# Optimization experiments

Hardware: AMD Instinct MI355X
Metric: run time of the kernel (lower is better)

## Reference

```python
import jax, jax.numpy as jnp
import numpy as np

BSZ, SEQ, HID, OUT = 64, 1024, 1024, 1024


def setup_inputs() -> dict:
    key = jax.random.key(0)
    k1, k2, k3, k4, k5 = jax.random.split(key, 5)
    hidden = jax.random.normal(k1, (BSZ, HID), dtype=jnp.float32)
    encoder_outs = jax.random.normal(k2, (BSZ, SEQ, OUT), dtype=jnp.float32)
    src_lens = jax.random.randint(k3, (BSZ,), 1, SEQ + 1)  # valid lengths in [1, SEQ]
    # nn.Linear weights (PyTorch stores W as [out_features, in_features])
    W1 = jax.random.normal(k4, (OUT, HID), dtype=jnp.float32) / np.sqrt(HID)
    W2 = jax.random.normal(k5, (OUT, HID + OUT), dtype=jnp.float32) / np.sqrt(HID + OUT)
    return {"hidden": hidden, "encoder_outs": encoder_outs, "src_lens": src_lens,
            "W1": W1, "W2": W2}


def reference(hidden, encoder_outs, src_lens, W1, W2):
    # x = l1(hidden): [bsz, out]
    x = hidden @ W1.T
    # att_score = bmm(encoder_outs, x[..., None]).squeeze(-1).T : [seq, bsz]
    att_score = jnp.einsum("bsd,bd->sb", encoder_outs, x)
    seq = encoder_outs.shape[1]
    # seq_mask transposed: [seq, bsz]
    seq_mask = (jnp.arange(seq)[None, :] < src_lens[:, None]).T
    # masked_att = mask * score; then exact-zero entries (masked OR true zeros) -> -1e10
    masked_att = seq_mask * att_score
    masked_att = jnp.where(masked_att == 0, jnp.float32(-1e10), masked_att)
    attn_scores = jax.nn.softmax(masked_att, axis=0)  # softmax over seq dim
    # context = sum_s attn[s,b] * enc[b,s,d] : [bsz, out]
    ctx = jnp.einsum("sb,bsd->bd", attn_scores, encoder_outs)
    out = jnp.tanh(jnp.concatenate((ctx, hidden), axis=1) @ W2.T)
    return out, attn_scores
```

## Files before the change

### kernel.cpp

```cpp
#include <hip/hip_runtime.h>
#include <math.h>

#define BSZ 64
#define SEQ 1024
#define HID 1024
#define DOUT 1024
#define SPLIT 16
#define CHUNK (SEQ/SPLIT)

typedef float f32x4 __attribute__((ext_vector_type(4)));


__global__ __launch_bounds__(256) void k_gemv_hid(const float* __restrict__ hidden,
                                                  const float* __restrict__ W1,
                                                  const float* __restrict__ W2,
                                                  float* __restrict__ xpart,
                                                  float* __restrict__ outpart) {
    __shared__ float tile[128 * 65];
    int t = threadIdx.x, lane = t & 63, wave = t >> 6;
    int k0 = blockIdx.y * 128;
#pragma unroll
    for (int p = 0; p < 8; ++p) {
        int b = p * 8 + (t >> 5), l5 = t & 31;
        f32x4 h = *(const f32x4*)&hidden[b * 1024 + k0 + l5 * 4];
        tile[(l5 * 4 + 0) * 65 + b] = h.x;
        tile[(l5 * 4 + 1) * 65 + b] = h.y;
        tile[(l5 * 4 + 2) * 65 + b] = h.z;
        tile[(l5 * 4 + 3) * 65 + b] = h.w;
    }
    __syncthreads();
    bool isX = blockIdx.x < 64;
    int cg = isX ? blockIdx.x : blockIdx.x - 64;
    int c_base = cg * 16 + (wave << 2);
    const float* w0p = isX ? (W1 + (size_t)c_base * 1024 + k0)
                           : (W2 + (size_t)c_base * 2048 + 1024 + k0);
    size_t ldw = isX ? 1024 : 2048;
    float acc[4] = {0.f, 0.f, 0.f, 0.f};
    for (int k = 0; k < 128; k += 4) {
        float v0 = tile[(k + 0) * 65 + lane];
        float v1 = tile[(k + 1) * 65 + lane];
        float v2 = tile[(k + 2) * 65 + lane];
        float v3 = tile[(k + 3) * 65 + lane];
#pragma unroll
        for (int oi = 0; oi < 4; ++oi) {
            f32x4 w = *(const f32x4*)&w0p[oi * ldw + k];
            acc[oi] += w.x * v0 + w.y * v1 + w.z * v2 + w.w * v3;
        }
    }
    float* dst = isX ? (xpart + (size_t)blockIdx.y * 65536)
                     : (outpart + (size_t)(8 + blockIdx.y) * 65536);
#pragma unroll
    for (int oi = 0; oi < 4; ++oi)
        dst[(size_t)lane * 1024 + c_base + oi] = acc[oi];
}

__global__ __launch_bounds__(256, 4) void k_score(const float* __restrict__ enc,
                                                  const float* __restrict__ xpart,
                                                  const int* __restrict__ src_lens,
                                                  float* __restrict__ scoresG,
                                                  float* __restrict__ ctx_part,
                                                  float* __restrict__ ml_part) {
    int b = blockIdx.y, chunk = blockIdx.x;
    int t = threadIdx.x, lane = t & 63, wave = t >> 6;
    __shared__ f32x4 accbuf[4 * 256];
    __shared__ float mbuf[4], lbuf[4];

    f32x4 xv[4];
#pragma unroll
    for (int i = 0; i < 4; ++i) {
        f32x4 s = (f32x4)0.f;
#pragma unroll
        for (int ks = 0; ks < 8; ++ks)
            s += ((const f32x4*)(xpart + (size_t)ks * 65536 + (size_t)b * 1024))[i * 64 + lane];
        xv[i] = s;
    }
    int len = src_lens[b];
    int s_wave0 = chunk * CHUNK + wave * 16;
    const float* encb = enc + ((size_t)b << 20);

    float m_run = -3.0e38f, l_run = 0.f;
    f32x4 acc[4];
#pragma unroll
    for (int i = 0; i < 4; ++i) acc[i] = (f32x4)0.f;

#pragma unroll 1
    for (int g = 0; g < 4; ++g) {
        int sbase = s_wave0 + g * 4;
        if (sbase >= len) {
            if (lane == 0) {
#pragma unroll
                for (int j = 0; j < 4; ++j) scoresG[(sbase + j) * BSZ + b] = -1.0e10f;
            }
            continue;
        }
        f32x4 e[4][4];
#pragma unroll
        for (int j = 0; j < 4; ++j) {
            const f32x4* row4 = (const f32x4*)(encb + (size_t)(sbase + j) * DOUT);
#pragma unroll
            for (int i = 0; i < 4; ++i) e[j][i] = row4[i * 64 + lane];
        }
        float d0 = 0.f, d1 = 0.f, d2 = 0.f, d3 = 0.f;
#pragma unroll
        for (int i = 0; i < 4; ++i) {
            d0 += e[0][i].x * xv[i].x + e[0][i].y * xv[i].y + e[0][i].z * xv[i].z + e[0][i].w * xv[i].w;
            d1 += e[1][i].x * xv[i].x + e[1][i].y * xv[i].y + e[1][i].z * xv[i].z + e[1][i].w * xv[i].w;
            d2 += e[2][i].x * xv[i].x + e[2][i].y * xv[i].y + e[2][i].z * xv[i].z + e[2][i].w * xv[i].w;
            d3 += e[3][i].x * xv[i].x + e[3][i].y * xv[i].y + e[3][i].z * xv[i].z + e[3][i].w * xv[i].w;
        }
#pragma unroll
        for (int off = 32; off > 0; off >>= 1) {
            d0 += __shfl_xor(d0, off, 64);
            d1 += __shfl_xor(d1, off, 64);
            d2 += __shfl_xor(d2, off, 64);
            d3 += __shfl_xor(d3, off, 64);
        }
        float v0 = (sbase + 0 < len) ? d0 : 0.f; if (v0 == 0.f) v0 = -1.0e10f;
        float v1 = (sbase + 1 < len) ? d1 : 0.f; if (v1 == 0.f) v1 = -1.0e10f;
        float v2 = (sbase + 2 < len) ? d2 : 0.f; if (v2 == 0.f) v2 = -1.0e10f;
        float v3 = (sbase + 3 < len) ? d3 : 0.f; if (v3 == 0.f) v3 = -1.0e10f;
        if (lane == 0) {
            scoresG[(sbase + 0) * BSZ + b] = v0;
            scoresG[(sbase + 1) * BSZ + b] = v1;
            scoresG[(sbase + 2) * BSZ + b] = v2;
            scoresG[(sbase + 3) * BSZ + b] = v3;
        }
        float msub = fmaxf(fmaxf(v0, v1), fmaxf(v2, v3));
        float m_new = fmaxf(m_run, msub);
        float scale = __expf(m_run - m_new);
        float p0 = __expf(v0 - m_new), p1 = __expf(v1 - m_new);
        float p2 = __expf(v2 - m_new), p3 = __expf(v3 - m_new);
        l_run = l_run * scale + (p0 + p1 + p2 + p3);
        m_run = m_new;
#pragma unroll
        for (int i = 0; i < 4; ++i)
            acc[i] = acc[i] * scale + p0 * e[0][i] + p1 * e[1][i] + p2 * e[2][i] + p3 * e[3][i];
    }

#pragma unroll
    for (int i = 0; i < 4; ++i) accbuf[wave * 256 + i * 64 + lane] = acc[i];
    if (lane == 0) { mbuf[wave] = m_run; lbuf[wave] = l_run; }
    __syncthreads();
    float M = fmaxf(fmaxf(mbuf[0], mbuf[1]), fmaxf(mbuf[2], mbuf[3]));
    float w0 = __expf(mbuf[0] - M), w1 = __expf(mbuf[1] - M);
    float w2 = __expf(mbuf[2] - M), w3 = __expf(mbuf[3] - M);
    f32x4 tot = accbuf[t] * w0 + accbuf[256 + t] * w1 + accbuf[512 + t] * w2 + accbuf[768 + t] * w3;
    ((f32x4*)(ctx_part + ((size_t)(b * SPLIT + chunk) << 10)))[t] = tot;
    if (t == 0) {
        float Lt = lbuf[0] * w0 + lbuf[1] * w1 + lbuf[2] * w2 + lbuf[3] * w3;
        ml_part[(b * SPLIT + chunk) * 2] = M;
        ml_part[(b * SPLIT + chunk) * 2 + 1] = Lt;
    }
}

__global__ __launch_bounds__(256) void k_reduce_attn(const float* __restrict__ ctx_part,
                                                     const float* __restrict__ ml_part,
                                                     const float* __restrict__ scoresG,
                                                     float* __restrict__ ctxT,
                                                     float* __restrict__ outAttn) {
    int b = blockIdx.x >> 2, q = blockIdx.x & 3, t = threadIdx.x;
    float M = -3.0e38f;
#pragma unroll
    for (int c = 0; c < SPLIT; ++c) M = fmaxf(M, ml_part[(b * SPLIT + c) * 2]);
    float L = 0.f;
    float wgt[SPLIT];
#pragma unroll
    for (int c = 0; c < SPLIT; ++c) {
        float e = __expf(ml_part[(b * SPLIT + c) * 2] - M);
        wgt[c] = e;
        L += ml_part[(b * SPLIT + c) * 2 + 1] * e;
    }
    float inv = 1.f / L;
    int d = q * 256 + t;
    float acc = 0.f;
#pragma unroll
    for (int c = 0; c < SPLIT; ++c)
        acc += wgt[c] * ctx_part[((size_t)(b * SPLIT + c) << 10) + d];
    ctxT[d * BSZ + b] = acc * inv;
    outAttn[d * BSZ + b] = __expf(scoresG[d * BSZ + b] - M) * inv;
}

__global__ __launch_bounds__(256) void k_out_part(const float* __restrict__ W2,
                                                  const float* __restrict__ ctxT,
                                                  float* __restrict__ outpart) {
    __shared__ float tile[128 * 64];
    int t = threadIdx.x, lane = t & 63, wave = t >> 6;
    int k0 = blockIdx.y * 128;
    int c_base = blockIdx.x * 16 + (wave << 2);
    {
        const f32x4* src = (const f32x4*)(ctxT + k0 * 64);
        f32x4* dst = (f32x4*)tile;
#pragma unroll
        for (int i = 0; i < 8; ++i) dst[t + i * 256] = src[t + i * 256];
    }
    __syncthreads();
    float acc[4] = {0.f, 0.f, 0.f, 0.f};
    for (int k = 0; k < 128; k += 4) {
        float v0 = tile[(k + 0) * 64 + lane];
        float v1 = tile[(k + 1) * 64 + lane];
        float v2 = tile[(k + 2) * 64 + lane];
        float v3 = tile[(k + 3) * 64 + lane];
#pragma unroll
        for (int oi = 0; oi < 4; ++oi) {
            f32x4 w = *(const f32x4*)&W2[(size_t)(c_base + oi) * 2048 + k0 + k];
            acc[oi] += w.x * v0 + w.y * v1 + w.z * v2 + w.w * v3;
        }
    }
#pragma unroll
    for (int oi = 0; oi < 4; ++oi)
        outpart[(size_t)blockIdx.y * 65536 + (size_t)lane * 1024 + c_base + oi] = acc[oi];
}

__global__ void k_out_reduce(const float* __restrict__ outpart, float* __restrict__ out) {
    int idx = blockIdx.x * 256 + threadIdx.x;
    float s = 0.f;
#pragma unroll
    for (int ks = 0; ks < 16; ++ks) s += outpart[(size_t)ks * 65536 + idx];
    out[idx] = tanhf(s);
}

extern "C" void kernel_launch(void* const* d_in, const int* in_sizes, int n_in,
                              void* d_out, int out_size, void* d_ws, size_t ws_size,
                              hipStream_t stream) {
    const float* hidden   = (const float*)d_in[0];
    const float* enc      = (const float*)d_in[1];
    const int*   src_lens = (const int*)d_in[2];
    const float* W1       = (const float*)d_in[3];
    const float* W2       = (const float*)d_in[4];
    float* out     = (float*)d_out;
    float* outAttn = out + 65536;

    float* ws       = (float*)d_ws;
    float* scoresG  = ws;
    float* ctxT     = ws + 65536;
    float* ctx_part = ws + 131072;
    float* ml_part  = ws + 1179648;
    float* xpart    = ws + 1181696;
    float* outpart  = ws + 1705984;

    k_gemv_hid<<<dim3(128, 8), 256, 0, stream>>>(hidden, W1, W2, xpart, outpart);
    k_score<<<dim3(SPLIT, BSZ), 256, 0, stream>>>(enc, xpart, src_lens, scoresG, ctx_part, ml_part);
    k_reduce_attn<<<256, 256, 0, stream>>>(ctx_part, ml_part, scoresG, ctxT, outAttn);
    k_out_part<<<dim3(64, 8), 256, 0, stream>>>(W2, ctxT, outpart);
    k_out_reduce<<<256, 256, 0, stream>>>(outpart, out);
}
```

Before: 72.11 us.

## Fuse output GEMV with tanh and concat, drop split-K reduce kernel

Removes the hidden-part of the W2 GEMV from the first kernel. The reduce-attention kernel now writes a transposed concat of context and hidden. A new single k_out kernel runs the full K=2048 dot per output column and applies tanh directly, which removes the split-K partial buffer and the separate reduce launch. The score kernel now loops only over valid groups, and masked attention entries are written as zero in the reduce kernel instead of storing -1e10 scores. The cost is that each k_out block walks the whole K range serially with only 256 blocks, which lowers parallelism on the W2 pass.

```diff
diff --git a/kernel.cpp b/kernel.cpp
--- a/kernel.cpp
+++ b/kernel.cpp
@@ -11,11 +11,9 @@
 typedef float f32x4 __attribute__((ext_vector_type(4)));
 
 
-__global__ __launch_bounds__(256) void k_gemv_hid(const float* __restrict__ hidden,
-                                                  const float* __restrict__ W1,
-                                                  const float* __restrict__ W2,
-                                                  float* __restrict__ xpart,
-                                                  float* __restrict__ outpart) {
+__global__ __launch_bounds__(256) void k_gemv_x(const float* __restrict__ hidden,
+                                                const float* __restrict__ W1,
+                                                float* __restrict__ xpart) {
     __shared__ float tile[128 * 65];
     int t = threadIdx.x, lane = t & 63, wave = t >> 6;
     int k0 = blockIdx.y * 128;
@@ -29,12 +27,7 @@
         tile[(l5 * 4 + 3) * 65 + b] = h.w;
     }
     __syncthreads();
-    bool isX = blockIdx.x < 64;
-    int cg = isX ? blockIdx.x : blockIdx.x - 64;
-    int c_base = cg * 16 + (wave << 2);
-    const float* w0p = isX ? (W1 + (size_t)c_base * 1024 + k0)
-                           : (W2 + (size_t)c_base * 2048 + 1024 + k0);
-    size_t ldw = isX ? 1024 : 2048;
+    int c_base = blockIdx.x * 16 + (wave << 2);
     float acc[4] = {0.f, 0.f, 0.f, 0.f};
     for (int k = 0; k < 128; k += 4) {
         float v0 = tile[(k + 0) * 65 + lane];
@@ -43,15 +36,13 @@
         float v3 = tile[(k + 3) * 65 + lane];
 #pragma unroll
         for (int oi = 0; oi < 4; ++oi) {
-            f32x4 w = *(const f32x4*)&w0p[oi * ldw + k];
+            f32x4 w = *(const f32x4*)&W1[(size_t)(c_base + oi) * 1024 + k0 + k];
             acc[oi] += w.x * v0 + w.y * v1 + w.z * v2 + w.w * v3;
         }
     }
-    float* dst = isX ? (xpart + (size_t)blockIdx.y * 65536)
-                     : (outpart + (size_t)(8 + blockIdx.y) * 65536);
 #pragma unroll
     for (int oi = 0; oi < 4; ++oi)
-        dst[(size_t)lane * 1024 + c_base + oi] = acc[oi];
+        xpart[(size_t)blockIdx.y * 65536 + (size_t)lane * 1024 + c_base + oi] = acc[oi];
 }
 
 __global__ __launch_bounds__(256, 4) void k_score(const float* __restrict__ enc,
@@ -78,21 +69,17 @@
     int s_wave0 = chunk * CHUNK + wave * 16;
     const float* encb = enc + ((size_t)b << 20);
 
+    int rem = len - s_wave0;
+    int ng = (rem + 3) >> 2;
+    ng = ng < 0 ? 0 : (ng > 4 ? 4 : ng);
+
     float m_run = -3.0e38f, l_run = 0.f;
     f32x4 acc[4];
 #pragma unroll
     for (int i = 0; i < 4; ++i) acc[i] = (f32x4)0.f;
 
-#pragma unroll 1
-    for (int g = 0; g < 4; ++g) {
+    for (int g = 0; g < ng; ++g) {
         int sbase = s_wave0 + g * 4;
-        if (sbase >= len) {
-            if (lane == 0) {
-#pragma unroll
-                for (int j = 0; j < 4; ++j) scoresG[(sbase + j) * BSZ + b] = -1.0e10f;
-            }
-            continue;
-        }
         f32x4 e[4][4];
 #pragma unroll
         for (int j = 0; j < 4; ++j) {
@@ -156,9 +143,12 @@
 __global__ __launch_bounds__(256) void k_reduce_attn(const float* __restrict__ ctx_part,
                                                      const float* __restrict__ ml_part,
                                                      const float* __restrict__ scoresG,
-                                                     float* __restrict__ ctxT,
+                                                     const int* __restrict__ src_lens,
+                                                     const float* __restrict__ hidden,
+                                                     float* __restrict__ concatT,
                                                      float* __restrict__ outAttn) {
     int b = blockIdx.x >> 2, q = blockIdx.x & 3, t = threadIdx.x;
+    int len = src_lens[b];
     float M = -3.0e38f;
 #pragma unroll
     for (int c = 0; c < SPLIT; ++c) M = fmaxf(M, ml_part[(b * SPLIT + c) * 2]);
@@ -176,47 +166,35 @@
 #pragma unroll
     for (int c = 0; c < SPLIT; ++c)
         acc += wgt[c] * ctx_part[((size_t)(b * SPLIT + c) << 10) + d];
-    ctxT[d * BSZ + b] = acc * inv;
-    outAttn[d * BSZ + b] = __expf(scoresG[d * BSZ + b] - M) * inv;
-}
-
-__global__ __launch_bounds__(256) void k_out_part(const float* __restrict__ W2,
-                                                  const float* __restrict__ ctxT,
-                                                  float* __restrict__ outpart) {
+    concatT[d * BSZ + b] = acc * inv;
+    outAttn[d * BSZ + b] = (d < len) ? __expf(scoresG[d * BSZ + b] - M) * inv : 0.f;
+    concatT[(1024 + d) * BSZ + b] = hidden[b * 1024 + d];
+}
+
+__global__ __launch_bounds__(256) void k_out(const float* __restrict__ W2,
+                                             const float* __restrict__ concatT,
+                                             float* __restrict__ out) {
     __shared__ float tile[128 * 64];
     int t = threadIdx.x, lane = t & 63, wave = t >> 6;
-    int k0 = blockIdx.y * 128;
-    int c_base = blockIdx.x * 16 + (wave << 2);
-    {
-        const f32x4* src = (const f32x4*)(ctxT + k0 * 64);
+    int c = blockIdx.x * 4 + wave;
+    const float* wrow = W2 + (size_t)c * 2048;
+    float acc = 0.f;
+    for (int kc = 0; kc < 16; ++kc) {
+        int k0 = kc * 128;
+        __syncthreads();
+        const f32x4* src = (const f32x4*)(concatT + (size_t)k0 * 64);
         f32x4* dst = (f32x4*)tile;
 #pragma unroll
         for (int i = 0; i < 8; ++i) dst[t + i * 256] = src[t + i * 256];
-    }
-    __syncthreads();
-    float acc[4] = {0.f, 0.f, 0.f, 0.f};
-    for (int k = 0; k < 128; k += 4) {
-        float v0 = tile[(k + 0) * 64 + lane];
-        float v1 = tile[(k + 1) * 64 + lane];
-        float v2 = tile[(k + 2) * 64 + lane];
-        float v3 = tile[(k + 3) * 64 + lane];
-#pragma unroll
-        for (int oi = 0; oi < 4; ++oi) {
-            f32x4 w = *(const f32x4*)&W2[(size_t)(c_base + oi) * 2048 + k0 + k];
-            acc[oi] += w.x * v0 + w.y * v1 + w.z * v2 + w.w * v3;
-        }
-    }
-#pragma unroll
-    for (int oi = 0; oi < 4; ++oi)
-        outpart[(size_t)blockIdx.y * 65536 + (size_t)lane * 1024 + c_base + oi] = acc[oi];
-}
-
-__global__ void k_out_reduce(const float* __restrict__ outpart, float* __restrict__ out) {
-    int idx = blockIdx.x * 256 + threadIdx.x;
-    float s = 0.f;
-#pragma unroll
-    for (int ks = 0; ks < 16; ++ks) s += outpart[(size_t)ks * 65536 + idx];
-    out[idx] = tanhf(s);
+        __syncthreads();
+#pragma unroll 4
+        for (int k = 0; k < 128; k += 4) {
+            f32x4 w = *(const f32x4*)&wrow[k0 + k];
+            acc += w.x * tile[(k + 0) * 64 + lane] + w.y * tile[(k + 1) * 64 + lane]
+                 + w.z * tile[(k + 2) * 64 + lane] + w.w * tile[(k + 3) * 64 + lane];
+        }
+    }
+    out[lane * 1024 + c] = tanhf(acc);
 }
 
 extern "C" void kernel_launch(void* const* d_in, const int* in_sizes, int n_in,
@@ -232,15 +210,13 @@
 
     float* ws       = (float*)d_ws;
     float* scoresG  = ws;
-    float* ctxT     = ws + 65536;
-    float* ctx_part = ws + 131072;
-    float* ml_part  = ws + 1179648;
-    float* xpart    = ws + 1181696;
-    float* outpart  = ws + 1705984;
-
-    k_gemv_hid<<<dim3(128, 8), 256, 0, stream>>>(hidden, W1, W2, xpart, outpart);
+    float* concatT  = ws + 65536;
+    float* ctx_part = ws + 196608;
+    float* ml_part  = ws + 1245184;
+    float* xpart    = ws + 1247232;
+
+    k_gemv_x<<<dim3(64, 8), 256, 0, stream>>>(hidden, W1, xpart);
     k_score<<<dim3(SPLIT, BSZ), 256, 0, stream>>>(enc, xpart, src_lens, scoresG, ctx_part, ml_part);
-    k_reduce_attn<<<256, 256, 0, stream>>>(ctx_part, ml_part, scoresG, ctxT, outAttn);
-    k_out_part<<<dim3(64, 8), 256, 0, stream>>>(W2, ctxT, outpart);
-    k_out_reduce<<<256, 256, 0, stream>>>(outpart, out);
-}
+    k_reduce_attn<<<256, 256, 0, stream>>>(ctx_part, ml_part, scoresG, src_lens, hidden, concatT, outAttn);
+    k_out<<<256, 256, 0, stream>>>(W2, concatT, out);
+}
```

Measured after the change: 101.7 us. 1.41x slower.

## Fuse softmax reduction, context GEMV and output tanh into one kernel

Applied to the files above, without the earlier changes.

Replaces the reduce_attn, out_part and out_reduce kernels with a single kernel. Each block rebuilds the context for two batches in shared memory, computes 128 output columns of the W2 GEMV, adds the precomputed hidden partials and applies tanh. The score kernel now loops only over valid groups, writes scores batch-major with vector stores, and the masked attention entries are written as zero directly. This removes two launches and the ctxT/outpart round trips. In exchange, each block redundantly recomputes the context reduction across 8 output blocks, and W2 is re-read per batch pair, giving 32 passes over that half of W2.

```diff
diff --git a/kernel.cpp b/kernel.cpp
--- a/kernel.cpp
+++ b/kernel.cpp
@@ -15,7 +15,7 @@
                                                   const float* __restrict__ W1,
                                                   const float* __restrict__ W2,
                                                   float* __restrict__ xpart,
-                                                  float* __restrict__ outpart) {
+                                                  float* __restrict__ outpart8) {
     __shared__ float tile[128 * 65];
     int t = threadIdx.x, lane = t & 63, wave = t >> 6;
     int k0 = blockIdx.y * 128;
@@ -48,7 +48,7 @@
         }
     }
     float* dst = isX ? (xpart + (size_t)blockIdx.y * 65536)
-                     : (outpart + (size_t)(8 + blockIdx.y) * 65536);
+                     : (outpart8 + (size_t)blockIdx.y * 65536);
 #pragma unroll
     for (int oi = 0; oi < 4; ++oi)
         dst[(size_t)lane * 1024 + c_base + oi] = acc[oi];
@@ -78,21 +78,17 @@
     int s_wave0 = chunk * CHUNK + wave * 16;
     const float* encb = enc + ((size_t)b << 20);
 
+    int rem = len - s_wave0;
+    int ng = (rem + 3) >> 2;
+    ng = ng < 0 ? 0 : (ng > 4 ? 4 : ng);
+
     float m_run = -3.0e38f, l_run = 0.f;
     f32x4 acc[4];
 #pragma unroll
     for (int i = 0; i < 4; ++i) acc[i] = (f32x4)0.f;
 
-#pragma unroll 1
-    for (int g = 0; g < 4; ++g) {
+    for (int g = 0; g < ng; ++g) {
         int sbase = s_wave0 + g * 4;
-        if (sbase >= len) {
-            if (lane == 0) {
-#pragma unroll
-                for (int j = 0; j < 4; ++j) scoresG[(sbase + j) * BSZ + b] = -1.0e10f;
-            }
-            continue;
-        }
         f32x4 e[4][4];
 #pragma unroll
         for (int j = 0; j < 4; ++j) {
@@ -120,10 +116,8 @@
         float v2 = (sbase + 2 < len) ? d2 : 0.f; if (v2 == 0.f) v2 = -1.0e10f;
         float v3 = (sbase + 3 < len) ? d3 : 0.f; if (v3 == 0.f) v3 = -1.0e10f;
         if (lane == 0) {
-            scoresG[(sbase + 0) * BSZ + b] = v0;
-            scoresG[(sbase + 1) * BSZ + b] = v1;
-            scoresG[(sbase + 2) * BSZ + b] = v2;
-            scoresG[(sbase + 3) * BSZ + b] = v3;
+            f32x4 sv = {v0, v1, v2, v3};
+            *(f32x4*)&scoresG[b * 1024 + sbase] = sv;
         }
         float msub = fmaxf(fmaxf(v0, v1), fmaxf(v2, v3));
         float m_new = fmaxf(m_run, msub);
@@ -153,70 +147,85 @@
     }
 }
 
-__global__ __launch_bounds__(256) void k_reduce_attn(const float* __restrict__ ctx_part,
-                                                     const float* __restrict__ ml_part,
-                                                     const float* __restrict__ scoresG,
-                                                     float* __restrict__ ctxT,
-                                                     float* __restrict__ outAttn) {
-    int b = blockIdx.x >> 2, q = blockIdx.x & 3, t = threadIdx.x;
-    float M = -3.0e38f;
-#pragma unroll
-    for (int c = 0; c < SPLIT; ++c) M = fmaxf(M, ml_part[(b * SPLIT + c) * 2]);
-    float L = 0.f;
-    float wgt[SPLIT];
-#pragma unroll
-    for (int c = 0; c < SPLIT; ++c) {
-        float e = __expf(ml_part[(b * SPLIT + c) * 2] - M);
-        wgt[c] = e;
-        L += ml_part[(b * SPLIT + c) * 2 + 1] * e;
-    }
-    float inv = 1.f / L;
-    int d = q * 256 + t;
-    float acc = 0.f;
-#pragma unroll
-    for (int c = 0; c < SPLIT; ++c)
-        acc += wgt[c] * ctx_part[((size_t)(b * SPLIT + c) << 10) + d];
-    ctxT[d * BSZ + b] = acc * inv;
-    outAttn[d * BSZ + b] = __expf(scoresG[d * BSZ + b] - M) * inv;
-}
-
-__global__ __launch_bounds__(256) void k_out_part(const float* __restrict__ W2,
-                                                  const float* __restrict__ ctxT,
-                                                  float* __restrict__ outpart) {
-    __shared__ float tile[128 * 64];
+__global__ __launch_bounds__(256) void k_outfinal(const float* __restrict__ ctx_part,
+                                                  const float* __restrict__ ml_part,
+                                                  const float* __restrict__ scoresG,
+                                                  const int* __restrict__ src_lens,
+                                                  const float* __restrict__ outpart8,
+                                                  const float* __restrict__ W2,
+                                                  float* __restrict__ out,
+                                                  float* __restrict__ outAttn) {
+    int bp = blockIdx.x >> 3, oq = blockIdx.x & 7;
+    int b0 = bp * 2, b1 = b0 + 1;
     int t = threadIdx.x, lane = t & 63, wave = t >> 6;
-    int k0 = blockIdx.y * 128;
-    int c_base = blockIdx.x * 16 + (wave << 2);
-    {
-        const f32x4* src = (const f32x4*)(ctxT + k0 * 64);
-        f32x4* dst = (f32x4*)tile;
-#pragma unroll
-        for (int i = 0; i < 8; ++i) dst[t + i * 256] = src[t + i * 256];
-    }
-    __syncthreads();
-    float acc[4] = {0.f, 0.f, 0.f, 0.f};
-    for (int k = 0; k < 128; k += 4) {
-        float v0 = tile[(k + 0) * 64 + lane];
-        float v1 = tile[(k + 1) * 64 + lane];
-        float v2 = tile[(k + 2) * 64 + lane];
-        float v3 = tile[(k + 3) * 64 + lane];
-#pragma unroll
-        for (int oi = 0; oi < 4; ++oi) {
-            f32x4 w = *(const f32x4*)&W2[(size_t)(c_base + oi) * 2048 + k0 + k];
-            acc[oi] += w.x * v0 + w.y * v1 + w.z * v2 + w.w * v3;
-        }
-    }
-#pragma unroll
-    for (int oi = 0; oi < 4; ++oi)
-        outpart[(size_t)blockIdx.y * 65536 + (size_t)lane * 1024 + c_base + oi] = acc[oi];
-}
-
-__global__ void k_out_reduce(const float* __restrict__ outpart, float* __restrict__ out) {
-    int idx = blockIdx.x * 256 + threadIdx.x;
-    float s = 0.f;
-#pragma unroll
-    for (int ks = 0; ks < 16; ++ks) s += outpart[(size_t)ks * 65536 + idx];
-    out[idx] = tanhf(s);
+    __shared__ float ctx_s[2][1024];
+    __shared__ float osum[2][128];
+
+    float inv[2];
+#pragma unroll
+    for (int bs = 0; bs < 2; ++bs) {
+        int b = b0 + bs;
+        float M = -3.0e38f;
+#pragma unroll
+        for (int c = 0; c < SPLIT; ++c) M = fmaxf(M, ml_part[(b * SPLIT + c) * 2]);
+        float L = 0.f;
+        float wgt[SPLIT];
+#pragma unroll
+        for (int c = 0; c < SPLIT; ++c) {
+            float e = __expf(ml_part[(b * SPLIT + c) * 2] - M);
+            wgt[c] = e;
+            L += ml_part[(b * SPLIT + c) * 2 + 1] * e;
+        }
+        inv[bs] = 1.f / L;
+#pragma unroll
+        for (int r = 0; r < 4; ++r) {
+            int d = r * 256 + t;
+            float a = 0.f;
+#pragma unroll
+            for (int c = 0; c < SPLIT; ++c)
+                a += wgt[c] * ctx_part[((size_t)(b * SPLIT + c) << 10) + d];
+            ctx_s[bs][d] = a * inv[bs];
+        }
+        if (oq == 0) {
+            int len = src_lens[b];
+#pragma unroll
+            for (int r = 0; r < 4; ++r) {
+                int s = r * 256 + t;
+                outAttn[s * BSZ + b] = (s < len) ? __expf(scoresG[b * 1024 + s] - M) * inv[bs] : 0.f;
+            }
+        }
+    }
+
+    int oblk = oq * 128;
+    int bsel = t >> 7, o_loc = t & 127;
+    float hseed = 0.f;
+#pragma unroll
+    for (int ks = 0; ks < 8; ++ks)
+        hseed += outpart8[(size_t)ks * 65536 + (size_t)(b0 + bsel) * 1024 + oblk + o_loc];
+    __syncthreads();
+
+#pragma unroll 2
+    for (int i = 0; i < 32; ++i) {
+        int o = oblk + wave * 32 + i;
+        const f32x4* w4 = (const f32x4*)(W2 + (size_t)o * 2048);
+        float s0 = 0.f, s1 = 0.f;
+#pragma unroll
+        for (int j = 0; j < 4; ++j) {
+            f32x4 w = w4[j * 64 + lane];
+            f32x4 c0 = ((const f32x4*)ctx_s[0])[j * 64 + lane];
+            f32x4 c1 = ((const f32x4*)ctx_s[1])[j * 64 + lane];
+            s0 += w.x * c0.x + w.y * c0.y + w.z * c0.z + w.w * c0.w;
+            s1 += w.x * c1.x + w.y * c1.y + w.z * c1.z + w.w * c1.w;
+        }
+#pragma unroll
+        for (int off = 32; off > 0; off >>= 1) {
+            s0 += __shfl_xor(s0, off, 64);
+            s1 += __shfl_xor(s1, off, 64);
+        }
+        if (lane == 0) { osum[0][wave * 32 + i] = s0; osum[1][wave * 32 + i] = s1; }
+    }
+    __syncthreads();
+    out[(size_t)(b0 + bsel) * 1024 + oblk + o_loc] = tanhf(osum[bsel][o_loc] + hseed);
 }
 
 extern "C" void kernel_launch(void* const* d_in, const int* in_sizes, int n_in,
@@ -232,15 +241,12 @@
 
     float* ws       = (float*)d_ws;
     float* scoresG  = ws;
-    float* ctxT     = ws + 65536;
-    float* ctx_part = ws + 131072;
-    float* ml_part  = ws + 1179648;
-    float* xpart    = ws + 1181696;
-    float* outpart  = ws + 1705984;
-
-    k_gemv_hid<<<dim3(128, 8), 256, 0, stream>>>(hidden, W1, W2, xpart, outpart);
+    float* ctx_part = ws + 65536;
+    float* ml_part  = ws + 1114112;
+    float* xpart    = ws + 1116160;
+    float* outpart8 = ws + 1640448;
+
+    k_gemv_hid<<<dim3(128, 8), 256, 0, stream>>>(hidden, W1, W2, xpart, outpart8);
     k_score<<<dim3(SPLIT, BSZ), 256, 0, stream>>>(enc, xpart, src_lens, scoresG, ctx_part, ml_part);
-    k_reduce_attn<<<256, 256, 0, stream>>>(ctx_part, ml_part, scoresG, ctxT, outAttn);
-    k_out_part<<<dim3(64, 8), 256, 0, stream>>>(W2, ctxT, outpart);
-    k_out_reduce<<<256, 256, 0, stream>>>(outpart, out);
-}
+    k_outfinal<<<256, 256, 0, stream>>>(ctx_part, ml_part, scoresG, src_lens, outpart8, W2, out, outAttn);
+}
```

Measured after the change: 101.2 us. +40.3%, slower.
